# Kernel tuning notes

Measured on AMD Instinct MI355X. Metric: run time of the kernel, lower is better.

The kernel has to match this reference:

```python
import jax, jax.numpy as jnp
import numpy as np

N = 1_000_000   # num nodes (num_node_G2)
D = 128         # embedding_dim
S = 2048        # sample_num
K = 128         # negative_sample_number
R2 = 1000       # num_relation_G2
R1 = 100        # num_relation_G1_sub1
GAMMA = 12.0


def setup_inputs() -> dict:
    key = jax.random.key(0)
    ks = jax.random.split(key, 24)
    ri = lambda k, shape, hi: jax.random.randint(k, shape, 0, hi, dtype=jnp.int32)
    inp = {
        "all_node_embedding": jax.random.normal(ks[0], (N, D), jnp.float32),
        "relation_embedding_G2": jax.random.normal(ks[1], (R2, D), jnp.float32),
        "relation_embedding_G1_ty_ty": jax.random.normal(ks[2], (R1, D), jnp.float32),
        "relation_embedding_G1_type_of": jax.random.normal(ks[3], (D,), jnp.float32),
        "head_idx_1": ri(ks[4], (S,), N),
        "rel_idx_1": ri(ks[5], (S,), R2),
        "tail_idx_1": ri(ks[6], (S,), N),
        "neg_tail_idx_1": ri(ks[7], (S, K), N),
        "neg_head_idx_1": ri(ks[8], (S, K), N),
        "head_idx_2": ri(ks[9], (S,), N),
        "rel_idx_2": ri(ks[10], (S,), R1),
        "tail_idx_2": ri(ks[11], (S,), N),
        "neg_tail_idx_2": ri(ks[12], (S, K), N),
        "neg_head_idx_2": ri(ks[13], (S, K), N),
        "head_idx_3": ri(ks[14], (S,), N),
        "tail_idx_3": ri(ks[15], (S,), N),
        "neg_tail_idx_3": ri(ks[16], (S, K), N),
        "neg_head_idx_3": ri(ks[17], (S, K), N),
    }
    return inp


def _part_scores(emb, h_idx, r, t_idx, nt_idx, nh_idx):
    """TransE L1 scores: positive [S,1], tail-corrupted [S,K], head-corrupted [S,K]."""
    h = emb[h_idx]                     # [S, D]
    t = emb[t_idx]                     # [S, D]
    pos = GAMMA - jnp.abs(h + r - t).sum(-1, keepdims=True)          # [S, 1]
    t_neg = emb[nt_idx]                # [S, K, D]
    neg_tail = GAMMA - jnp.abs((h + r)[:, None, :] - t_neg).sum(-1)  # [S, K]
    h_neg = emb[nh_idx]                # [S, K, D]  (head-match: h_neg + (r - t))
    neg_head = GAMMA - jnp.abs(h_neg + (r - t)[:, None, :]).sum(-1)  # [S, K]
    return pos, neg_tail, neg_head


def reference(all_node_embedding, relation_embedding_G2, relation_embedding_G1_ty_ty,
              relation_embedding_G1_type_of,
              head_idx_1, rel_idx_1, tail_idx_1, neg_tail_idx_1, neg_head_idx_1,
              head_idx_2, rel_idx_2, tail_idx_2, neg_tail_idx_2, neg_head_idx_2,
              head_idx_3, tail_idx_3, neg_tail_idx_3, neg_head_idx_3):
    r1 = relation_embedding_G2[rel_idx_1]                 # [S, D]
    p1, nt1, nh1 = _part_scores(all_node_embedding, head_idx_1, r1, tail_idx_1,
                                neg_tail_idx_1, neg_head_idx_1)
    r2 = relation_embedding_G1_ty_ty[rel_idx_2]           # [S, D]
    p2, nt2, nh2 = _part_scores(all_node_embedding, head_idx_2, r2, tail_idx_2,
                                neg_tail_idx_2, neg_head_idx_2)
    r3 = jnp.broadcast_to(relation_embedding_G1_type_of, (head_idx_3.shape[0], D))
    p3, nt3, nh3 = _part_scores(all_node_embedding, head_idx_3, r3, tail_idx_3,
                                neg_tail_idx_3, neg_head_idx_3)
    return (p1, nt1, nh1, p2, nt2, nh2, p3, nt3, nh3)
```

## Files before the change

kernel.cpp:

```cpp
#include <hip/hip_runtime.h>

#define DIM 128
#define SAMP 2048
#define KNEG 128
#define GAMMA 12.0f

__global__ __launch_bounds__(256) void transe_score_kernel(
    const float* __restrict__ emb,
    const float* __restrict__ relG2,
    const float* __restrict__ relG1,
    const float* __restrict__ relTO,
    const int* __restrict__ head1, const int* __restrict__ rel1,
    const int* __restrict__ tail1, const int* __restrict__ nt1,
    const int* __restrict__ nh1,
    const int* __restrict__ head2, const int* __restrict__ rel2,
    const int* __restrict__ tail2, const int* __restrict__ nt2,
    const int* __restrict__ nh2,
    const int* __restrict__ head3, const int* __restrict__ tail3,
    const int* __restrict__ nt3, const int* __restrict__ nh3,
    float* __restrict__ out)
{
    const int s    = blockIdx.x;
    const int part = blockIdx.y;
    const int tid  = threadIdx.x;
    const int lane = tid & 63;
    const int wid  = tid >> 6;
    const int half = (lane >> 5);
    const int l32  = lane & 31;

    __shared__ __align__(16) float hr[DIM];
    __shared__ __align__(16) float rt[DIM];
    __shared__ float posbuf[DIM];

    const int* hidx; const int* tidx; const int* ntidx; const int* nhidx;
    const float* rrow;
    if (part == 0)      { hidx=head1; tidx=tail1; ntidx=nt1; nhidx=nh1; rrow = relG2 + (long)rel1[s]*DIM; }
    else if (part == 1) { hidx=head2; tidx=tail2; ntidx=nt2; nhidx=nh2; rrow = relG1 + (long)rel2[s]*DIM; }
    else                { hidx=head3; tidx=tail3; ntidx=nt3; nhidx=nh3; rrow = relTO; }

    const int h = hidx[s];
    const int t = tidx[s];

    if (tid < DIM) {
        float hv = emb[(long)h*DIM + tid];
        float rv = rrow[tid];
        float tv = emb[(long)t*DIM + tid];
        float a  = hv + rv;
        hr[tid] = a;
        rt[tid] = rv - tv;
        posbuf[tid] = fabsf(a - tv);
    }
    __syncthreads();

    const long P       = (long)SAMP + 2L*SAMP*KNEG;
    const long pos_off = (long)part * P;
    const long nt_off  = pos_off + SAMP;
    const long nh_off  = nt_off + (long)SAMP*KNEG;

    if (wid == 0) {
        float v = posbuf[lane] + posbuf[lane + 64];
        #pragma unroll
        for (int off = 32; off; off >>= 1) v += __shfl_down(v, off, 64);
        if (lane == 0) out[pos_off + s] = GAMMA - v;
    }

    const float4 hrv = ((const float4*)hr)[l32];
    const float4 rtv = ((const float4*)rt)[l32];

    #pragma unroll 4
    for (int iter = 0; iter < 32; ++iter) {
        const int r = iter * 8 + wid * 2 + half;
        const bool isTail = (r < KNEG);
        const int j = isTail ? r : r - KNEG;
        const int idx = isTail ? ntidx[s*KNEG + j] : nhidx[s*KNEG + j];
        const float4 e = ((const float4*)(emb + (long)idx * DIM))[l32];

        float sum;
        if (isTail) {
            sum = fabsf(hrv.x - e.x) + fabsf(hrv.y - e.y)
                + fabsf(hrv.z - e.z) + fabsf(hrv.w - e.w);
        } else {
            sum = fabsf(e.x + rtv.x) + fabsf(e.y + rtv.y)
                + fabsf(e.z + rtv.z) + fabsf(e.w + rtv.w);
        }
        #pragma unroll
        for (int off = 16; off; off >>= 1) sum += __shfl_down(sum, off, 32);
        if (l32 == 0) {
            const long o = isTail ? (nt_off + (long)s*KNEG + j)
                                  : (nh_off + (long)s*KNEG + j);
            out[o] = GAMMA - sum;
        }
    }
}

extern "C" void kernel_launch(void* const* d_in, const int* in_sizes, int n_in,
                              void* d_out, int out_size, void* d_ws, size_t ws_size,
                              hipStream_t stream) {
    const float* emb   = (const float*)d_in[0];
    const float* relG2 = (const float*)d_in[1];
    const float* relG1 = (const float*)d_in[2];
    const float* relTO = (const float*)d_in[3];
    const int* head1 = (const int*)d_in[4];
    const int* rel1  = (const int*)d_in[5];
    const int* tail1 = (const int*)d_in[6];
    const int* nt1   = (const int*)d_in[7];
    const int* nh1   = (const int*)d_in[8];
    const int* head2 = (const int*)d_in[9];
    const int* rel2  = (const int*)d_in[10];
    const int* tail2 = (const int*)d_in[11];
    const int* nt2   = (const int*)d_in[12];
    const int* nh2   = (const int*)d_in[13];
    const int* head3 = (const int*)d_in[14];
    const int* tail3 = (const int*)d_in[15];
    const int* nt3   = (const int*)d_in[16];
    const int* nh3   = (const int*)d_in[17];
    float* out = (float*)d_out;

    dim3 grid(SAMP, 3);
    dim3 block(256);
    transe_score_kernel<<<grid, block, 0, stream>>>(
        emb, relG2, relG1, relTO,
        head1, rel1, tail1, nt1, nh1,
        head2, rel2, tail2, nt2, nh2,
        head3, tail3, nt3, nh3,
        out);
}
```

Before: 723.7 us.

## Stage negative indices and scores in shared memory, split tail/head loops

All 256 negative indices for a sample are now loaded cooperatively into shared memory up front, so the gather loop no longer does per-iteration dependent global index loads. The tail and head loops are separated and fully unrolled, which removes the branch and lets many row gathers be in flight at once. Scores are buffered in shared memory and written out as coalesced stores instead of scattered single-lane writes. An occupancy hint of 8 blocks per multiprocessor is added, which may limit registers available to the unrolled loops.

```diff
diff --git a/kernel.cpp b/kernel.cpp
--- a/kernel.cpp
+++ b/kernel.cpp
@@ -5,7 +5,7 @@
 #define KNEG 128
 #define GAMMA 12.0f
 
-__global__ __launch_bounds__(256) void transe_score_kernel(
+__global__ __launch_bounds__(256, 8) void transe_score_kernel(
     const float* __restrict__ emb,
     const float* __restrict__ relG2,
     const float* __restrict__ relG1,
@@ -27,10 +27,13 @@
     const int wid  = tid >> 6;
     const int half = (lane >> 5);
     const int l32  = lane & 31;
+    const int c    = wid * 2 + half;
 
     __shared__ __align__(16) float hr[DIM];
     __shared__ __align__(16) float rt[DIM];
     __shared__ float posbuf[DIM];
+    __shared__ int   idxbuf[2 * KNEG];
+    __shared__ float scorebuf[2 * KNEG];
 
     const int* hidx; const int* tidx; const int* ntidx; const int* nhidx;
     const float* rrow;
@@ -38,10 +41,12 @@
     else if (part == 1) { hidx=head2; tidx=tail2; ntidx=nt2; nhidx=nh2; rrow = relG1 + (long)rel2[s]*DIM; }
     else                { hidx=head3; tidx=tail3; ntidx=nt3; nhidx=nh3; rrow = relTO; }
 
-    const int h = hidx[s];
-    const int t = tidx[s];
+    const int sK = s * KNEG;
 
     if (tid < DIM) {
+        idxbuf[tid] = ntidx[sK + tid];
+        const int h = hidx[s];
+        const int t = tidx[s];
         float hv = emb[(long)h*DIM + tid];
         float rv = rrow[tid];
         float tv = emb[(long)t*DIM + tid];
@@ -49,6 +54,8 @@
         hr[tid] = a;
         rt[tid] = rv - tv;
         posbuf[tid] = fabsf(a - tv);
+    } else {
+        idxbuf[tid] = nhidx[sK + tid - KNEG];
     }
     __syncthreads();
 
@@ -67,30 +74,33 @@
     const float4 hrv = ((const float4*)hr)[l32];
     const float4 rtv = ((const float4*)rt)[l32];
 
-    #pragma unroll 4
-    for (int iter = 0; iter < 32; ++iter) {
-        const int r = iter * 8 + wid * 2 + half;
-        const bool isTail = (r < KNEG);
-        const int j = isTail ? r : r - KNEG;
-        const int idx = isTail ? ntidx[s*KNEG + j] : nhidx[s*KNEG + j];
+    #pragma unroll
+    for (int it = 0; it < 16; ++it) {
+        const int j = it * 8 + c;
+        const int idx = idxbuf[j];
         const float4 e = ((const float4*)(emb + (long)idx * DIM))[l32];
-
-        float sum;
-        if (isTail) {
-            sum = fabsf(hrv.x - e.x) + fabsf(hrv.y - e.y)
-                + fabsf(hrv.z - e.z) + fabsf(hrv.w - e.w);
-        } else {
-            sum = fabsf(e.x + rtv.x) + fabsf(e.y + rtv.y)
-                + fabsf(e.z + rtv.z) + fabsf(e.w + rtv.w);
-        }
+        float sum = fabsf(hrv.x - e.x) + fabsf(hrv.y - e.y)
+                  + fabsf(hrv.z - e.z) + fabsf(hrv.w - e.w);
         #pragma unroll
         for (int off = 16; off; off >>= 1) sum += __shfl_down(sum, off, 32);
-        if (l32 == 0) {
-            const long o = isTail ? (nt_off + (long)s*KNEG + j)
-                                  : (nh_off + (long)s*KNEG + j);
-            out[o] = GAMMA - sum;
-        }
+        if (l32 == 0) scorebuf[j] = GAMMA - sum;
     }
+
+    #pragma unroll
+    for (int it = 0; it < 16; ++it) {
+        const int j = it * 8 + c;
+        const int idx = idxbuf[KNEG + j];
+        const float4 e = ((const float4*)(emb + (long)idx * DIM))[l32];
+        float sum = fabsf(e.x + rtv.x) + fabsf(e.y + rtv.y)
+                  + fabsf(e.z + rtv.z) + fabsf(e.w + rtv.w);
+        #pragma unroll
+        for (int off = 16; off; off >>= 1) sum += __shfl_down(sum, off, 32);
+        if (l32 == 0) scorebuf[KNEG + j] = GAMMA - sum;
+    }
+    __syncthreads();
+
+    if (tid < KNEG) out[nt_off + sK + tid] = scorebuf[tid];
+    else            out[nh_off + sK + tid - KNEG] = scorebuf[tid];
 }
 
 extern "C" void kernel_launch(void* const* d_in, const int* in_sizes, int n_in,
```

New measurement: 697.5 us. 1.04x faster.
